# Kernel tuning notes

Measured on AMD Instinct MI355X. Metric: run time of the kernel, lower is better.

The kernel has to match this reference:

```python
import jax, jax.numpy as jnp
import numpy as np

N_NODES = 15135


def setup_inputs() -> dict:
    key = jax.random.key(0)
    ks = jax.random.split(key, 12)
    bs, N, F_in, H, L, Hfc, C, E = 8, N_NODES, 64, 128, 3, 512, 10, 242160
    s = lambda k, *sh: jax.random.normal(k, sh, dtype=jnp.float32) * 0.05
    return {
        "x": jax.random.normal(ks[0], (bs, N, F_in), dtype=jnp.float32),
        "edge_index": jax.random.randint(ks[1], (2, E), 0, N),
        "W1": s(ks[2], F_in, H), "b1": jnp.zeros((H,), jnp.float32),
        "W2": s(ks[3], H, H),   "b2": jnp.zeros((H,), jnp.float32),
        "W3": s(ks[4], H, H),   "b3": jnp.zeros((H,), jnp.float32),
        "Wfc": s(ks[5], L * H, 1), "bfc": jnp.zeros((1,), jnp.float32),
        "Wl1": s(ks[6], N, Hfc), "bl1": jnp.zeros((Hfc,), jnp.float32),
        "Wl2": s(ks[7], Hfc, C), "bl2": jnp.zeros((C,), jnp.float32),
    }


def _gcn_norm(edge_index, num_nodes):
    # add self loops, compute symmetric normalization (PyG GCNConv default)
    loop = jnp.arange(num_nodes, dtype=edge_index.dtype)
    src = jnp.concatenate([edge_index[0], loop])
    dst = jnp.concatenate([edge_index[1], loop])
    deg = jax.ops.segment_sum(jnp.ones_like(dst, dtype=jnp.float32), dst,
                              num_segments=num_nodes)
    dinv = jax.lax.rsqrt(deg)  # deg >= 1 due to self-loops
    norm = dinv[src] * dinv[dst]
    return src, dst, norm


def _gcn_conv(x, W, b, src, dst, norm):
    # x: [bs, N, Fin] -> [bs, N, Fout]
    xl = jnp.einsum("bnf,fh->bnh", x, W)
    msg = xl[:, src, :] * norm[None, :, None]  # [bs, E+N, Fout]
    out = jnp.zeros_like(xl).at[:, dst].add(msg)
    return out + b


def reference(x, edge_index, W1, b1, W2, b2, W3, b3, Wfc, bfc, Wl1, bl1, Wl2, bl2):
    bs, N, _ = x.shape
    src, dst, norm = _gcn_norm(edge_index, N)
    h1 = jax.nn.relu(_gcn_conv(x, W1, b1, src, dst, norm))
    h2 = jax.nn.relu(_gcn_conv(h1, W2, b2, src, dst, norm))
    h3 = jax.nn.relu(_gcn_conv(h2, W3, b3, src, dst, norm))
    # mode='cat': torch.stack(xs, -1).view(bs, N, -1) interleaves features
    hcat = jnp.stack([h1, h2, h3], axis=-1).reshape(bs, N, -1)  # [bs,N,H*L]
    g = (jnp.einsum("bnk,ko->bno", hcat, Wfc) + bfc).reshape(bs, N)
    # dropout layers are identity in eval mode
    z = jax.nn.relu(g @ Wl1 + bl1)
    logits = z @ Wl2 + bl2
    return jax.nn.log_softmax(logits, axis=-1)
```

## Files before the change

### kernel.cpp

```cpp
#include <hip/hip_runtime.h>
#include <hip/hip_bf16.h>

#define NN 15135
#define BS 8
#define FIN 64
#define HD 128
#define EE 242160
#define HFC 512
#define NCLS 10

#define M_ROWS (BS * NN)
#define M_PAD  121088
#define PADE   348160
#define NT4    3784

#define NCH 237
#define NPLANES (NCH * 2)

typedef __attribute__((ext_vector_type(8))) short bf16x8;
typedef __attribute__((ext_vector_type(4))) float f32x4;

__device__ __forceinline__ unsigned short to_bf16(float f) {
    unsigned u = __float_as_uint(f);
    u = (u + 0x7fffu + ((u >> 16) & 1u)) >> 16;
    return (unsigned short)u;
}
__device__ __forceinline__ unsigned pack2_bf16(float lo, float hi) {
    unsigned a = __float_as_uint(lo);
    unsigned b = __float_as_uint(hi);
    a = (a + 0x7fffu + ((a >> 16) & 1u)) >> 16;
    b = (b + 0x7fffu + ((b >> 16) & 1u)) & 0xffff0000u;
    return (a & 0xffffu) | b;
}

__global__ void k_deg(const int* __restrict__ dst, int* __restrict__ degi) {
    int e = blockIdx.x * 256 + threadIdx.x;
    if (e < EE) atomicAdd(&degi[dst[e]], 1);
}

#define SCAN_T 1024
#define SCAN_PER 15
__global__ __launch_bounds__(SCAN_T) void k_scan(const int* __restrict__ degi,
                                                 int* __restrict__ row_ptr,
                                                 float* __restrict__ dinv) {
    __shared__ int part[SCAN_T];
    const int t = threadIdx.x;
    const int base = t * SCAN_PER;
    int loc[SCAN_PER];
    int s = 0;
#pragma unroll
    for (int i = 0; i < SCAN_PER; i++) {
        int d = (base + i < NN) ? degi[base + i] : 0;
        if (base + i < NN) dinv[base + i] = rsqrtf((float)d + 1.0f);
        int pd = (d + 7) & ~7;
        loc[i] = s; s += pd;
    }
    part[t] = s;
    __syncthreads();
    for (int off = 1; off < SCAN_T; off <<= 1) {
        int v = (t >= off) ? part[t - off] : 0;
        __syncthreads();
        part[t] += v;
        __syncthreads();
    }
    int before = (t == 0) ? 0 : part[t - 1];
#pragma unroll
    for (int i = 0; i < SCAN_PER; i++)
        if (base + i < NN) row_ptr[base + i] = before + loc[i];
    if (t == SCAN_T - 1) row_ptr[NN] = part[SCAN_T - 1];
}

__global__ void k_bucket(const int* __restrict__ src, const int* __restrict__ dst,
                         const int* __restrict__ row_ptr, int* __restrict__ cursor,
                         const float* __restrict__ dinv,
                         int* __restrict__ s_idx, float* __restrict__ wts) {
    int e = blockIdx.x * 256 + threadIdx.x;
    if (e >= EE) return;
    int s = src[e], d = dst[e];
    int pos = atomicAdd(&cursor[d], 1);
    int idx = row_ptr[d] + pos;
    s_idx[idx] = s;
    wts[idx] = dinv[s] * dinv[d];
}

__global__ void k_cvtW(const float* __restrict__ W1, const float* __restrict__ W2,
                       const float* __restrict__ W3, unsigned short* __restrict__ Wt) {
    int idx = blockIdx.x * 256 + threadIdx.x;
    const float* W; int K, base;
    if (idx < 8192)       { W = W1; K = 64;  base = idx; }
    else if (idx < 24576) { W = W2; K = 128; base = idx - 8192; }
    else                  { W = W3; K = 128; base = idx - 24576; }
    int c = base / K, k = base % K;
    Wt[idx] = to_bf16(W[(size_t)k * HD + c]);
}

__global__ __launch_bounds__(256) void k_aggx(const float* __restrict__ x,
                                              const int* __restrict__ rp,
                                              const int* __restrict__ s_idx,
                                              const float* __restrict__ wts,
                                              const float* __restrict__ dinv,
                                              unsigned short* __restrict__ Ab) {
    const int tid = threadIdx.x;
    const int widx = tid >> 6, lane = tid & 63;
    const int bid = blockIdx.x;
    const int bb = bid & 7;
    const int n = (bid >> 3) * 4 + widx;
    if (n >= NN) return;
    const float* Xs = x + (size_t)bb * NN * FIN;

    const int e0 = __builtin_amdgcn_readfirstlane(rp[n]);
    const int e1 = __builtin_amdgcn_readfirstlane(rp[n + 1]);
    const float dv = dinv[n];
    float acc0 = dv * dv * Xs[(size_t)n * FIN + lane];
    float acc1 = 0.f;

    for (int c = e0; c < e1; c += 8) {
        int s0 = s_idx[c + 0], s1 = s_idx[c + 1], s2 = s_idx[c + 2], s3 = s_idx[c + 3];
        int s4 = s_idx[c + 4], s5 = s_idx[c + 5], s6 = s_idx[c + 6], s7 = s_idx[c + 7];
        float w0 = wts[c + 0], w1 = wts[c + 1], w2 = wts[c + 2], w3 = wts[c + 3];
        float w4 = wts[c + 4], w5 = wts[c + 5], w6 = wts[c + 6], w7 = wts[c + 7];
        float u0 = Xs[(size_t)s0 * FIN + lane];
        float u1 = Xs[(size_t)s1 * FIN + lane];
        float u2 = Xs[(size_t)s2 * FIN + lane];
        float u3 = Xs[(size_t)s3 * FIN + lane];
        float u4 = Xs[(size_t)s4 * FIN + lane];
        float u5 = Xs[(size_t)s5 * FIN + lane];
        float u6 = Xs[(size_t)s6 * FIN + lane];
        float u7 = Xs[(size_t)s7 * FIN + lane];
        acc0 += w0 * u0; acc1 += w1 * u1;
        acc0 += w2 * u2; acc1 += w3 * u3;
        acc0 += w4 * u4; acc1 += w5 * u5;
        acc0 += w6 * u6; acc1 += w7 * u7;
    }
    Ab[(size_t)bb * NN * FIN + (size_t)n * FIN + lane] = to_bf16(acc0 + acc1);
}

__global__ __launch_bounds__(256) void k_agg128(const unsigned short* __restrict__ Xb,
                                                const int* __restrict__ rp,
                                                const int* __restrict__ s_idx,
                                                const float* __restrict__ wts,
                                                const float* __restrict__ dinv,
                                                unsigned short* __restrict__ Ab) {
    const int tid = threadIdx.x;
    const int widx = tid >> 6, lane = tid & 63;
    const int bid = blockIdx.x;
    const int bb = bid & 7;
    const int n = (bid >> 3) * 4 + widx;
    if (n >= NN) return;
    const unsigned short* Xs = Xb + (size_t)bb * NN * HD + 2 * lane;

    const int e0 = __builtin_amdgcn_readfirstlane(rp[n]);
    const int e1 = __builtin_amdgcn_readfirstlane(rp[n + 1]);
    const float dv = dinv[n];

    float ax0, ay0, ax1 = 0.f, ay1 = 0.f;
    {
        unsigned u = *(const unsigned*)&Xs[(size_t)n * HD];
        float w0 = dv * dv;
        ax0 = w0 * __uint_as_float(u << 16);
        ay0 = w0 * __uint_as_float(u & 0xffff0000u);
    }
    for (int c = e0; c < e1; c += 8) {
        int s0 = s_idx[c + 0], s1 = s_idx[c + 1], s2 = s_idx[c + 2], s3 = s_idx[c + 3];
        int s4 = s_idx[c + 4], s5 = s_idx[c + 5], s6 = s_idx[c + 6], s7 = s_idx[c + 7];
        float w0 = wts[c + 0], w1 = wts[c + 1], w2 = wts[c + 2], w3 = wts[c + 3];
        float w4 = wts[c + 4], w5 = wts[c + 5], w6 = wts[c + 6], w7 = wts[c + 7];
        unsigned u0 = *(const unsigned*)&Xs[(size_t)s0 * HD];
        unsigned u1 = *(const unsigned*)&Xs[(size_t)s1 * HD];
        unsigned u2 = *(const unsigned*)&Xs[(size_t)s2 * HD];
        unsigned u3 = *(const unsigned*)&Xs[(size_t)s3 * HD];
        unsigned u4 = *(const unsigned*)&Xs[(size_t)s4 * HD];
        unsigned u5 = *(const unsigned*)&Xs[(size_t)s5 * HD];
        unsigned u6 = *(const unsigned*)&Xs[(size_t)s6 * HD];
        unsigned u7 = *(const unsigned*)&Xs[(size_t)s7 * HD];
        ax0 += w0 * __uint_as_float(u0 << 16); ay0 += w0 * __uint_as_float(u0 & 0xffff0000u);
        ax1 += w1 * __uint_as_float(u1 << 16); ay1 += w1 * __uint_as_float(u1 & 0xffff0000u);
        ax0 += w2 * __uint_as_float(u2 << 16); ay0 += w2 * __uint_as_float(u2 & 0xffff0000u);
        ax1 += w3 * __uint_as_float(u3 << 16); ay1 += w3 * __uint_as_float(u3 & 0xffff0000u);
        ax0 += w4 * __uint_as_float(u4 << 16); ay0 += w4 * __uint_as_float(u4 & 0xffff0000u);
        ax1 += w5 * __uint_as_float(u5 << 16); ay1 += w5 * __uint_as_float(u5 & 0xffff0000u);
        ax0 += w6 * __uint_as_float(u6 << 16); ay0 += w6 * __uint_as_float(u6 & 0xffff0000u);
        ax1 += w7 * __uint_as_float(u7 << 16); ay1 += w7 * __uint_as_float(u7 & 0xffff0000u);
    }
    *(unsigned*)&Ab[(size_t)bb * NN * HD + (size_t)n * HD + 2 * lane] =
        pack2_bf16(ax0 + ax1, ay0 + ay1);
}

template<int KD, int LIDX, bool GINIT, bool STOREH>
__global__ __launch_bounds__(256) void k_gemm_ep(const unsigned short* __restrict__ Xb,
                                                 const unsigned short* __restrict__ Wt,
                                                 const float* __restrict__ bias,
                                                 const float* __restrict__ Wfc,
                                                 const float* __restrict__ bfc,
                                                 unsigned short* __restrict__ H,
                                                 float* __restrict__ g) {
    constexpr int NK = KD / 32;
    const int tid = threadIdx.x;
    const int w = tid >> 6, lane = tid & 63;
    const int l15 = lane & 15, lhi = lane >> 4;
    const int row0 = blockIdx.x * 64;
    const int cbase = w * 32;

    bf16x8 B[2][NK];
#pragma unroll
    for (int ct = 0; ct < 2; ct++)
#pragma unroll
        for (int ks = 0; ks < NK; ks++)
            B[ct][ks] = *(const bf16x8*)&Wt[(size_t)(cbase + ct * 16 + l15) * KD + ks * 32 + lhi * 8];

    f32x4 acc[4][2] = {};
#pragma unroll
    for (int ks = 0; ks < NK; ks++) {
        bf16x8 A[4];
#pragma unroll
        for (int rt = 0; rt < 4; rt++)
            A[rt] = *(const bf16x8*)&Xb[(size_t)(row0 + rt * 16 + l15) * KD + ks * 32 + lhi * 8];
#pragma unroll
        for (int rt = 0; rt < 4; rt++)
#pragma unroll
            for (int ct = 0; ct < 2; ct++)
                acc[rt][ct] = __builtin_amdgcn_mfma_f32_16x16x32_bf16(A[rt], B[ct][ks], acc[rt][ct], 0, 0, 0);
    }

    __shared__ float gred[4][64];
    const float bias0 = bias[cbase + l15], bias1 = bias[cbase + 16 + l15];
    const float wf0 = Wfc[(cbase + l15) * 3 + LIDX];
    const float wf1 = Wfc[(cbase + 16 + l15) * 3 + LIDX];
#pragma unroll
    for (int rt = 0; rt < 4; rt++) {
#pragma unroll
        for (int reg = 0; reg < 4; reg++) {
            const int row = row0 + rt * 16 + lhi * 4 + reg;
            float h0 = fmaxf(acc[rt][0][reg] + bias0, 0.f);
            float h1 = fmaxf(acc[rt][1][reg] + bias1, 0.f);
            if (STOREH) {
                H[(size_t)row * 128 + cbase + l15] = to_bf16(h0);
                H[(size_t)row * 128 + cbase + 16 + l15] = to_bf16(h1);
            }
            float p = h0 * wf0 + h1 * wf1;
#pragma unroll
            for (int m = 8; m; m >>= 1) p += __shfl_xor(p, m, 64);
            if (l15 == 0) gred[w][rt * 16 + lhi * 4 + reg] = p;
        }
    }
    __syncthreads();
    if (tid < 64) {
        const int row = row0 + tid;
        if (row < M_ROWS) {
            float s = gred[0][tid] + gred[1][tid] + gred[2][tid] + gred[3][tid];
            if (GINIT) g[row] = bfc[0] + s; else g[row] += s;
        }
    }
}

__global__ __launch_bounds__(256) void k_fc1part(const float* __restrict__ g,
                                                 const float* __restrict__ Wl1,
                                                 float* __restrict__ part) {
    const int ct = threadIdx.x & 127;
    const int st = threadIdx.x >> 7;
    const int n0 = blockIdx.x * 64;
    __shared__ float gs[BS][64];
    for (int i = threadIdx.x; i < BS * 64; i += 256) {
        int b = i >> 6, j = i & 63;
        int n = n0 + j;
        gs[b][j] = (n < NN) ? g[b * NN + n] : 0.f;
    }
    __syncthreads();

    f32x4 acc[BS] = {};
    const int jend = (64 < NN - n0) ? 64 : NN - n0;
#pragma unroll 4
    for (int j = st; j < jend; j += 2) {
        f32x4 wv = *(const f32x4*)&Wl1[(size_t)(n0 + j) * HFC + 4 * ct];
#pragma unroll
        for (int b = 0; b < BS; b++) acc[b] += gs[b][j] * wv;
    }
    float* p = &part[((size_t)(blockIdx.x * 2 + st)) * (BS * HFC)];
#pragma unroll
    for (int b = 0; b < BS; b++)
        *(f32x4*)&p[b * HFC + 4 * ct] = acc[b];
}

__global__ __launch_bounds__(128) void k_fc1red(const float* __restrict__ part,
                                                const float* __restrict__ bl1,
                                                float* __restrict__ z) {
    const int idx = blockIdx.x * 128 + threadIdx.x;
    float s = 0.f;
#pragma unroll 8
    for (int y = 0; y < NPLANES; y++) s += part[(size_t)y * (BS * HFC) + idx];
    z[idx] = fmaxf(s + bl1[idx & 511], 0.f);
}

__global__ void k_head(const float* __restrict__ z, const float* __restrict__ Wl2,
                       const float* __restrict__ bl2, float* __restrict__ out) {
    __shared__ float lg[BS][NCLS];
    const int t = threadIdx.x;
    if (t < BS * NCLS) {
        int b = t / NCLS, c = t % NCLS;
        float a = bl2[c];
        for (int k = 0; k < HFC; k++) a += z[b * HFC + k] * Wl2[k * NCLS + c];
        lg[b][c] = a;
    }
    __syncthreads();
    if (t < BS * NCLS) {
        int b = t / NCLS, c = t % NCLS;
        float m = -1e30f;
#pragma unroll
        for (int j = 0; j < NCLS; j++) m = fmaxf(m, lg[b][j]);
        float s = 0.f;
#pragma unroll
        for (int j = 0; j < NCLS; j++) s += expf(lg[b][j] - m);
        out[b * NCLS + c] = lg[b][c] - m - logf(s);
    }
}

extern "C" void kernel_launch(void* const* d_in, const int* in_sizes, int n_in,
                              void* d_out, int out_size, void* d_ws, size_t ws_size,
                              hipStream_t stream) {
    const float* x   = (const float*)d_in[0];
    const int*   ei  = (const int*)d_in[1];
    const float* W1  = (const float*)d_in[2];
    const float* b1  = (const float*)d_in[3];
    const float* W2  = (const float*)d_in[4];
    const float* b2  = (const float*)d_in[5];
    const float* W3  = (const float*)d_in[6];
    const float* b3  = (const float*)d_in[7];
    const float* Wfc = (const float*)d_in[8];
    const float* bfc = (const float*)d_in[9];
    const float* Wl1 = (const float*)d_in[10];
    const float* bl1 = (const float*)d_in[11];
    const float* Wl2 = (const float*)d_in[12];
    const float* bl2 = (const float*)d_in[13];
    float* out = (float*)d_out;

    const int* srcp = ei;
    const int* dstp = ei + EE;

    float* ws = (float*)d_ws;
    float* dinv    = ws;
    float* g       = ws + 15360;
    float* z       = ws + 136448;
    float* part    = ws + 140544;
    int*   degi    = (int*)(ws + 2082048);
    int*   cursor  = (int*)(ws + 2097408);
    int*   row_ptr = (int*)(ws + 2112768);
    int*   s_idx   = (int*)(ws + 2128256);
    float* wts     = ws + 2476416;
    unsigned short* Wt  = (unsigned short*)(ws + 2824576);
    unsigned short* Wt1 = Wt;
    unsigned short* Wt2 = Wt + 8192;
    unsigned short* Wt3 = Wt + 24576;
    unsigned short* a0  = (unsigned short*)(ws + 2845056);
    unsigned short* B1  = (unsigned short*)(ws + 6719872);
    unsigned short* B2  = (unsigned short*)(ws + 14469504);

    const int gemm_grid = M_PAD / 64;

    hipMemsetAsync(degi, 0, 2 * 15360 * sizeof(int), stream);
    hipMemsetAsync(s_idx, 0, 2 * PADE * sizeof(int), stream);
    k_deg<<<(EE + 255) / 256, 256, 0, stream>>>(dstp, degi);
    k_scan<<<1, SCAN_T, 0, stream>>>(degi, row_ptr, dinv);
    k_bucket<<<(EE + 255) / 256, 256, 0, stream>>>(srcp, dstp, row_ptr, cursor, dinv, s_idx, wts);
    k_cvtW<<<160, 256, 0, stream>>>(W1, W2, W3, Wt);

    k_aggx<<<NT4 * 8, 256, 0, stream>>>(x, row_ptr, s_idx, wts, dinv, a0);
    k_gemm_ep<64, 0, true, true><<<gemm_grid, 256, 0, stream>>>(a0, Wt1, b1, Wfc, bfc, B1, g);
    k_agg128<<<NT4 * 8, 256, 0, stream>>>(B1, row_ptr, s_idx, wts, dinv, B2);
    k_gemm_ep<128, 1, false, true><<<gemm_grid, 256, 0, stream>>>(B2, Wt2, b2, Wfc, bfc, B1, g);
    k_agg128<<<NT4 * 8, 256, 0, stream>>>(B1, row_ptr, s_idx, wts, dinv, B2);
    k_gemm_ep<128, 2, false, false><<<gemm_grid, 256, 0, stream>>>(B2, Wt3, b3, Wfc, bfc, B1, g);

    k_fc1part<<<NCH, 256, 0, stream>>>(g, Wl1, part);
    k_fc1red<<<32, 128, 0, stream>>>(part, bl1, z);
    k_head<<<1, 128, 0, stream>>>(z, Wl2, bl2, out);
}
```

Baseline: 457.4 us.

## Pack CSR index and weight together and gather wide rows per lane group

Edge source indices and normalization weights move from two separate arrays into one interleaved int2 array, so each edge needs a single load. The aggregation kernels now split each wavefront into four 16-lane groups, each handling a different edge with 16-byte vector loads of the neighbor row, then combine the groups with cross-lane shuffles before the store. This cuts the number of load instructions and index/weight fetches per edge, at the cost of a shuffle reduction and only a quarter of the lanes doing the final store. Padding zeros in the CSR still act as zero-weight edges.

```diff
diff --git a/kernel.cpp b/kernel.cpp
--- a/kernel.cpp
+++ b/kernel.cpp
@@ -72,15 +72,12 @@
 
 __global__ void k_bucket(const int* __restrict__ src, const int* __restrict__ dst,
                          const int* __restrict__ row_ptr, int* __restrict__ cursor,
-                         const float* __restrict__ dinv,
-                         int* __restrict__ s_idx, float* __restrict__ wts) {
+                         const float* __restrict__ dinv, int2* __restrict__ csr) {
     int e = blockIdx.x * 256 + threadIdx.x;
     if (e >= EE) return;
     int s = src[e], d = dst[e];
     int pos = atomicAdd(&cursor[d], 1);
-    int idx = row_ptr[d] + pos;
-    s_idx[idx] = s;
-    wts[idx] = dinv[s] * dinv[d];
+    csr[row_ptr[d] + pos] = make_int2(s, __float_as_int(dinv[s] * dinv[d]));
 }
 
 __global__ void k_cvtW(const float* __restrict__ W1, const float* __restrict__ W2,
@@ -96,8 +93,7 @@
 
 __global__ __launch_bounds__(256) void k_aggx(const float* __restrict__ x,
                                               const int* __restrict__ rp,
-                                              const int* __restrict__ s_idx,
-                                              const float* __restrict__ wts,
+                                              const int2* __restrict__ csr,
                                               const float* __restrict__ dinv,
                                               unsigned short* __restrict__ Ab) {
     const int tid = threadIdx.x;
@@ -106,39 +102,43 @@
     const int bb = bid & 7;
     const int n = (bid >> 3) * 4 + widx;
     if (n >= NN) return;
-    const float* Xs = x + (size_t)bb * NN * FIN;
+    const int grp = lane >> 4;
+    const int l15 = lane & 15;
+    const float* Xs = x + (size_t)bb * NN * FIN + l15 * 4;
 
     const int e0 = __builtin_amdgcn_readfirstlane(rp[n]);
     const int e1 = __builtin_amdgcn_readfirstlane(rp[n + 1]);
     const float dv = dinv[n];
-    float acc0 = dv * dv * Xs[(size_t)n * FIN + lane];
-    float acc1 = 0.f;
-
+
+    f32x4 acc = {};
     for (int c = e0; c < e1; c += 8) {
-        int s0 = s_idx[c + 0], s1 = s_idx[c + 1], s2 = s_idx[c + 2], s3 = s_idx[c + 3];
-        int s4 = s_idx[c + 4], s5 = s_idx[c + 5], s6 = s_idx[c + 6], s7 = s_idx[c + 7];
-        float w0 = wts[c + 0], w1 = wts[c + 1], w2 = wts[c + 2], w3 = wts[c + 3];
-        float w4 = wts[c + 4], w5 = wts[c + 5], w6 = wts[c + 6], w7 = wts[c + 7];
-        float u0 = Xs[(size_t)s0 * FIN + lane];
-        float u1 = Xs[(size_t)s1 * FIN + lane];
-        float u2 = Xs[(size_t)s2 * FIN + lane];
-        float u3 = Xs[(size_t)s3 * FIN + lane];
-        float u4 = Xs[(size_t)s4 * FIN + lane];
-        float u5 = Xs[(size_t)s5 * FIN + lane];
-        float u6 = Xs[(size_t)s6 * FIN + lane];
-        float u7 = Xs[(size_t)s7 * FIN + lane];
-        acc0 += w0 * u0; acc1 += w1 * u1;
-        acc0 += w2 * u2; acc1 += w3 * u3;
-        acc0 += w4 * u4; acc1 += w5 * u5;
-        acc0 += w6 * u6; acc1 += w7 * u7;
-    }
-    Ab[(size_t)bb * NN * FIN + (size_t)n * FIN + lane] = to_bf16(acc0 + acc1);
+        int2 pA = csr[c + grp];
+        int2 pB = csr[c + 4 + grp];
+        float wA = __int_as_float(pA.y), wB = __int_as_float(pB.y);
+        f32x4 uA = *(const f32x4*)&Xs[(size_t)pA.x * FIN];
+        f32x4 uB = *(const f32x4*)&Xs[(size_t)pB.x * FIN];
+        acc += wA * uA;
+        acc += wB * uB;
+    }
+#pragma unroll
+    for (int j = 0; j < 4; j++) {
+        acc[j] += __shfl_xor(acc[j], 16, 64);
+        acc[j] += __shfl_xor(acc[j], 32, 64);
+    }
+    if (grp == 0) {
+        f32x4 vs = *(const f32x4*)&Xs[(size_t)n * FIN];
+        float w0 = dv * dv;
+        acc += w0 * vs;
+        uint2 st;
+        st.x = pack2_bf16(acc[0], acc[1]);
+        st.y = pack2_bf16(acc[2], acc[3]);
+        *(uint2*)&Ab[(size_t)bb * NN * FIN + (size_t)n * FIN + l15 * 4] = st;
+    }
 }
 
 __global__ __launch_bounds__(256) void k_agg128(const unsigned short* __restrict__ Xb,
                                                 const int* __restrict__ rp,
-                                                const int* __restrict__ s_idx,
-                                                const float* __restrict__ wts,
+                                                const int2* __restrict__ csr,
                                                 const float* __restrict__ dinv,
                                                 unsigned short* __restrict__ Ab) {
     const int tid = threadIdx.x;
@@ -147,43 +147,49 @@
     const int bb = bid & 7;
     const int n = (bid >> 3) * 4 + widx;
     if (n >= NN) return;
-    const unsigned short* Xs = Xb + (size_t)bb * NN * HD + 2 * lane;
+    const int grp = lane >> 4;
+    const int l15 = lane & 15;
+    const unsigned short* Xs = Xb + (size_t)bb * NN * HD + l15 * 8;
 
     const int e0 = __builtin_amdgcn_readfirstlane(rp[n]);
     const int e1 = __builtin_amdgcn_readfirstlane(rp[n + 1]);
     const float dv = dinv[n];
 
-    float ax0, ay0, ax1 = 0.f, ay1 = 0.f;
-    {
-        unsigned u = *(const unsigned*)&Xs[(size_t)n * HD];
+    float a[8] = {};
+    for (int c = e0; c < e1; c += 8) {
+        int2 pA = csr[c + grp];
+        int2 pB = csr[c + 4 + grp];
+        float wA = __int_as_float(pA.y), wB = __int_as_float(pB.y);
+        uint4 uA = *(const uint4*)&Xs[(size_t)pA.x * HD];
+        uint4 uB = *(const uint4*)&Xs[(size_t)pB.x * HD];
+#pragma unroll
+        for (int j = 0; j < 4; j++) {
+            unsigned vA = ((const unsigned*)&uA)[j];
+            unsigned vB = ((const unsigned*)&uB)[j];
+            a[2 * j + 0] += wA * __uint_as_float(vA << 16);
+            a[2 * j + 1] += wA * __uint_as_float(vA & 0xffff0000u);
+            a[2 * j + 0] += wB * __uint_as_float(vB << 16);
+            a[2 * j + 1] += wB * __uint_as_float(vB & 0xffff0000u);
+        }
+    }
+#pragma unroll
+    for (int j = 0; j < 8; j++) {
+        a[j] += __shfl_xor(a[j], 16, 64);
+        a[j] += __shfl_xor(a[j], 32, 64);
+    }
+    if (grp == 0) {
+        uint4 us = *(const uint4*)&Xs[(size_t)n * HD];
         float w0 = dv * dv;
-        ax0 = w0 * __uint_as_float(u << 16);
-        ay0 = w0 * __uint_as_float(u & 0xffff0000u);
-    }
-    for (int c = e0; c < e1; c += 8) {
-        int s0 = s_idx[c + 0], s1 = s_idx[c + 1], s2 = s_idx[c + 2], s3 = s_idx[c + 3];
-        int s4 = s_idx[c + 4], s5 = s_idx[c + 5], s6 = s_idx[c + 6], s7 = s_idx[c + 7];
-        float w0 = wts[c + 0], w1 = wts[c + 1], w2 = wts[c + 2], w3 = wts[c + 3];
-        float w4 = wts[c + 4], w5 = wts[c + 5], w6 = wts[c + 6], w7 = wts[c + 7];
-        unsigned u0 = *(const unsigned*)&Xs[(size_t)s0 * HD];
-        unsigned u1 = *(const unsigned*)&Xs[(size_t)s1 * HD];
-        unsigned u2 = *(const unsigned*)&Xs[(size_t)s2 * HD];
-        unsigned u3 = *(const unsigned*)&Xs[(size_t)s3 * HD];
-        unsigned u4 = *(const unsigned*)&Xs[(size_t)s4 * HD];
-        unsigned u5 = *(const unsigned*)&Xs[(size_t)s5 * HD];
-        unsigned u6 = *(const unsigned*)&Xs[(size_t)s6 * HD];
-        unsigned u7 = *(const unsigned*)&Xs[(size_t)s7 * HD];
-        ax0 += w0 * __uint_as_float(u0 << 16); ay0 += w0 * __uint_as_float(u0 & 0xffff0000u);
-        ax1 += w1 * __uint_as_float(u1 << 16); ay1 += w1 * __uint_as_float(u1 & 0xffff0000u);
-        ax0 += w2 * __uint_as_float(u2 << 16); ay0 += w2 * __uint_as_float(u2 & 0xffff0000u);
-        ax1 += w3 * __uint_as_float(u3 << 16); ay1 += w3 * __uint_as_float(u3 & 0xffff0000u);
-        ax0 += w4 * __uint_as_float(u4 << 16); ay0 += w4 * __uint_as_float(u4 & 0xffff0000u);
-        ax1 += w5 * __uint_as_float(u5 << 16); ay1 += w5 * __uint_as_float(u5 & 0xffff0000u);
-        ax0 += w6 * __uint_as_float(u6 << 16); ay0 += w6 * __uint_as_float(u6 & 0xffff0000u);
-        ax1 += w7 * __uint_as_float(u7 << 16); ay1 += w7 * __uint_as_float(u7 & 0xffff0000u);
-    }
-    *(unsigned*)&Ab[(size_t)bb * NN * HD + (size_t)n * HD + 2 * lane] =
-        pack2_bf16(ax0 + ax1, ay0 + ay1);
+        uint4 st;
+#pragma unroll
+        for (int j = 0; j < 4; j++) {
+            unsigned v = ((const unsigned*)&us)[j];
+            float lo = a[2 * j + 0] + w0 * __uint_as_float(v << 16);
+            float hi = a[2 * j + 1] + w0 * __uint_as_float(v & 0xffff0000u);
+            ((unsigned*)&st)[j] = pack2_bf16(lo, hi);
+        }
+        *(uint4*)&Ab[(size_t)bb * NN * HD + (size_t)n * HD + l15 * 8] = st;
+    }
 }
 
 template<int KD, int LIDX, bool GINIT, bool STOREH>
@@ -344,8 +350,7 @@
     int*   degi    = (int*)(ws + 2082048);
     int*   cursor  = (int*)(ws + 2097408);
     int*   row_ptr = (int*)(ws + 2112768);
-    int*   s_idx   = (int*)(ws + 2128256);
-    float* wts     = ws + 2476416;
+    int2*  csr     = (int2*)(ws + 2128256);
     unsigned short* Wt  = (unsigned short*)(ws + 2824576);
     unsigned short* Wt1 = Wt;
     unsigned short* Wt2 = Wt + 8192;
@@ -357,17 +362,17 @@
     const int gemm_grid = M_PAD / 64;
 
     hipMemsetAsync(degi, 0, 2 * 15360 * sizeof(int), stream);
-    hipMemsetAsync(s_idx, 0, 2 * PADE * sizeof(int), stream);
+    hipMemsetAsync(csr, 0, (size_t)PADE * 8, stream);
     k_deg<<<(EE + 255) / 256, 256, 0, stream>>>(dstp, degi);
     k_scan<<<1, SCAN_T, 0, stream>>>(degi, row_ptr, dinv);
-    k_bucket<<<(EE + 255) / 256, 256, 0, stream>>>(srcp, dstp, row_ptr, cursor, dinv, s_idx, wts);
+    k_bucket<<<(EE + 255) / 256, 256, 0, stream>>>(srcp, dstp, row_ptr, cursor, dinv, csr);
     k_cvtW<<<160, 256, 0, stream>>>(W1, W2, W3, Wt);
 
-    k_aggx<<<NT4 * 8, 256, 0, stream>>>(x, row_ptr, s_idx, wts, dinv, a0);
+    k_aggx<<<NT4 * 8, 256, 0, stream>>>(x, row_ptr, csr, dinv, a0);
     k_gemm_ep<64, 0, true, true><<<gemm_grid, 256, 0, stream>>>(a0, Wt1, b1, Wfc, bfc, B1, g);
-    k_agg128<<<NT4 * 8, 256, 0, stream>>>(B1, row_ptr, s_idx, wts, dinv, B2);
+    k_agg128<<<NT4 * 8, 256, 0, stream>>>(B1, row_ptr, csr, dinv, B2);
     k_gemm_ep<128, 1, false, true><<<gemm_grid, 256, 0, stream>>>(B2, Wt2, b2, Wfc, bfc, B1, g);
-    k_agg128<<<NT4 * 8, 256, 0, stream>>>(B1, row_ptr, s_idx, wts, dinv, B2);
+    k_agg128<<<NT4 * 8, 256, 0, stream>>>(B1, row_ptr, csr, dinv, B2);
     k_gemm_ep<128, 2, false, false><<<gemm_grid, 256, 0, stream>>>(B2, Wt3, b3, Wfc, bfc, B1, g);
 
     k_fc1part<<<NCH, 256, 0, stream>>>(g, Wl1, part);
```

New measurement: 484.3 us. +5.9%, slower.
